# Kernel optimization log

Hardware: AMD Instinct MI355X
Metric: run time of the kernel (lower is better)

## Reference

```python
import jax, jax.numpy as jnp
import numpy as np

B, F, H, E, O = 512, 512, 512, 8, 512  # batch, feature, hidden, experts, out_frame


def setup_inputs() -> dict:
    key = jax.random.key(0)
    ks = jax.random.split(key, 14)
    u = lambda k, shape, s: jax.random.uniform(k, shape, jnp.float32) * s
    return {
        "x": jax.random.normal(ks[0], (B, F), jnp.float32),
        # gating MLP params (torch Linear: y = x @ W.T + b)
        "gw0": u(ks[1], (H, F), 0.04) - 0.02,
        "gb0": jnp.zeros((H,), jnp.float32),
        "gw1": u(ks[2], (H, H), 0.04) - 0.02,
        "gb1": jnp.zeros((H,), jnp.float32),
        "gw2": u(ks[3], (E, H), 0.04) - 0.02,
        "gb2": jnp.zeros((E,), jnp.float32),
        # expert weight/bias banks
        "alpha0": u(ks[4], (E, H, F), 0.01),
        "beta0": jnp.zeros((E, H, 1), jnp.float32),
        "alpha1": u(ks[5], (E, H, H), 0.01),
        "beta1": jnp.zeros((E, H, 1), jnp.float32),
        "alpha2": u(ks[6], (E, O, H), 0.01),
        "beta2": jnp.zeros((E, O, 1), jnp.float32),
    }


def reference(x, gw0, gb0, gw1, gb1, gw2, gb2,
              alpha0, beta0, alpha1, beta1, alpha2, beta2):
    # gating network
    h = jax.nn.elu(x @ gw0.T + gb0)
    h = jax.nn.elu(h @ gw1.T + gb1)
    g = jax.nn.softmax(h @ gw2.T + gb2, axis=1)  # [B, E]

    # per-sample blended weights (sum over experts of gate-scaled expert mats)
    blend_w = lambda a: jnp.einsum('be,ehf->bhf', g, a)
    blend_b = lambda b: jnp.einsum('be,eh->bh', g, b[..., 0])

    # per-sample 3-layer MLP (bmm with vector rhs == batched matvec)
    H1 = jax.nn.elu(jnp.einsum('bhf,bf->bh', blend_w(alpha0), x) + blend_b(beta0))
    H2 = jax.nn.elu(jnp.einsum('bhf,bf->bh', blend_w(alpha1), H1) + blend_b(beta1))
    H3 = jnp.einsum('bof,bf->bo', blend_w(alpha2), H2) + blend_b(beta2)
    return H3
```

## Files before the change

### kernel.cpp

```cpp
#include <hip/hip_runtime.h>
#include <hip/hip_bf16.h>
#include <math.h>

enum { Bq = 512, Fq = 512, Hq = 512, Eq = 8, Oq = 512 };

typedef __attribute__((ext_vector_type(8))) short short8;
typedef __attribute__((ext_vector_type(4))) float floatx4;

static __device__ __forceinline__ unsigned short f2bf(float f) {
  unsigned u = __float_as_uint(f);
  u += 0x7fffu + ((u >> 16) & 1u);
  return (unsigned short)(u >> 16);
}
static __device__ __forceinline__ float bf2f(unsigned short h) {
  return __uint_as_float(((unsigned)h) << 16);
}
static __device__ __forceinline__ float elu1(float v) {
  return v > 0.f ? v : (__expf(v) - 1.f);
}

typedef __attribute__((address_space(1))) const unsigned int gu32;
typedef __attribute__((address_space(3))) unsigned int lu32;
static __device__ __forceinline__ void gld16(const unsigned short* g,
                                             unsigned short* l) {
  __builtin_amdgcn_global_load_lds((gu32*)g, (lu32*)l, 16, 0, 0);
}

static __device__ __forceinline__ int swz(int q, int r) {
  return (q & ~7) | ((q ^ r) & 7);
}

__global__ __launch_bounds__(256) void cvt6_kernel(
    const float* __restrict__ b0, const float* __restrict__ b1,
    const float* __restrict__ b2, unsigned short* __restrict__ db0,
    unsigned short* __restrict__ db1, unsigned short* __restrict__ db2,
    const float* __restrict__ s0, const float* __restrict__ s1,
    const float* __restrict__ s2, unsigned short* __restrict__ ds0,
    unsigned short* __restrict__ ds1, unsigned short* __restrict__ ds2,
    int nb, int ns) {
  int i = blockIdx.x * 256 + threadIdx.x;
  const float4* s;
  unsigned short* d;
  int j;
  if (i < 3 * nb) {
    int seg = i / nb;
    j = i - seg * nb;
    s = (seg == 0) ? (const float4*)b0
      : (seg == 1) ? (const float4*)b1 : (const float4*)b2;
    d = (seg == 0) ? db0 : (seg == 1) ? db1 : db2;
  } else {
    int k = i - 3 * nb;
    if (k >= 3 * ns) return;
    int seg = k / ns;
    j = k - seg * ns;
    s = (seg == 0) ? (const float4*)s0
      : (seg == 1) ? (const float4*)s1 : (const float4*)s2;
    d = (seg == 0) ? ds0 : (seg == 1) ? ds1 : ds2;
  }
  float4 v = s[j];
  ushort4 o;
  o.x = f2bf(v.x); o.y = f2bf(v.y); o.z = f2bf(v.z); o.w = f2bf(v.w);
  *(ushort4*)(d + 4 * (size_t)j) = o;
}

__global__ __launch_bounds__(256) void gating_gemm(
    const unsigned short* __restrict__ A, const unsigned short* __restrict__ W,
    const float* __restrict__ bias, unsigned short* __restrict__ C) {
  __shared__ unsigned short As[32 * 512];
  __shared__ unsigned short Ws[32 * 512];
  const int tid = threadIdx.x;
  const int wave = tid >> 6, lane = tid & 63;
  const int wm = wave >> 1, wn = wave & 1;
  const int lr = lane & 15, lk = lane >> 4;
  const int m0 = blockIdx.y * 32, n0 = blockIdx.x * 32;
#pragma unroll
  for (int i = 0; i < 8; i++) {
    int c = tid + i * 256;
    int r = c >> 6, ql = c & 63;
    gld16(&A[(size_t)(m0 + r) * 512 + swz(ql, r) * 8], &As[(c & ~63) * 8]);
  }
#pragma unroll
  for (int i = 0; i < 8; i++) {
    int c = tid + i * 256;
    int r = c >> 6, ql = c & 63;
    gld16(&W[(size_t)(n0 + r) * 512 + swz(ql, r) * 8], &Ws[(c & ~63) * 8]);
  }
  __syncthreads();
  const int rA = wm * 16 + lr, rB = wn * 16 + lr;
  floatx4 ac[4];
#pragma unroll
  for (int j = 0; j < 4; j++) ac[j] = (floatx4){0.f, 0.f, 0.f, 0.f};
#pragma unroll
  for (int t = 0; t < 4; t++) {
#pragma unroll
    for (int j = 0; j < 4; j++) {
      int q = ((j * 128 + t * 32) >> 3) + lk;
      short8 av = *(const short8*)&As[rA * 512 + swz(q, rA) * 8];
      short8 bv = *(const short8*)&Ws[rB * 512 + swz(q, rB) * 8];
      ac[j] = __builtin_amdgcn_mfma_f32_16x16x32_bf16(av, bv, ac[j], 0, 0, 0);
    }
  }
  floatx4 acc = (ac[0] + ac[1]) + (ac[2] + ac[3]);
  int n = n0 + wn * 16 + lr;
  float bn = bias[n];
#pragma unroll
  for (int r = 0; r < 4; r++) {
    int m = m0 + wm * 16 + lk * 4 + r;
    C[(size_t)m * 512 + n] = f2bf(elu1(acc[r] + bn));
  }
}

template <int FROMP>
__global__ __launch_bounds__(256) void expert_gemm(
    const unsigned short* __restrict__ A,
    const float* __restrict__ Pin,
    const unsigned short* __restrict__ Wb,
    const float* __restrict__ g,
    const float* __restrict__ beta,
    float* __restrict__ Pout) {
  __shared__ unsigned short As[32 * 256];
  __shared__ unsigned short Ws[2][32 * 256];
  const int tid = threadIdx.x;
  const int wave = tid >> 6, lane = tid & 63;
  const int wm = wave >> 1, wn = wave & 1;
  const int lr = lane & 15, lk = lane >> 4;
  const int m0 = blockIdx.y * 32, n0 = blockIdx.x * 32;
  const int kz = blockIdx.z, kbeg = kz * 256;

  if (FROMP) {
#pragma unroll
    for (int i = 0; i < 4; i++) {
      int c = tid + i * 256;
      int r = c >> 5, q = c & 31;
      const float* p0 = Pin + (size_t)(m0 + r) * 512 + kbeg + q * 8;
      const float* p1 = p0 + (size_t)Bq * Hq;
      float4 x0 = *(const float4*)p0, x1 = *(const float4*)(p0 + 4);
      float4 y0 = *(const float4*)p1, y1 = *(const float4*)(p1 + 4);
      short8 o;
      o[0] = (short)f2bf(elu1(x0.x + y0.x));
      o[1] = (short)f2bf(elu1(x0.y + y0.y));
      o[2] = (short)f2bf(elu1(x0.z + y0.z));
      o[3] = (short)f2bf(elu1(x0.w + y0.w));
      o[4] = (short)f2bf(elu1(x1.x + y1.x));
      o[5] = (short)f2bf(elu1(x1.y + y1.y));
      o[6] = (short)f2bf(elu1(x1.z + y1.z));
      o[7] = (short)f2bf(elu1(x1.w + y1.w));
      *(short8*)&As[(r * 32 + swz(q, r)) * 8] = o;
    }
  } else {
#pragma unroll
    for (int i = 0; i < 4; i++) {
      int c = tid + i * 256;
      int r = c >> 5, ql = c & 31;
      gld16(&A[(size_t)(m0 + r) * 512 + kbeg + swz(ql, r) * 8],
            &As[(c & ~63) * 8]);
    }
  }
#pragma unroll
  for (int i = 0; i < 4; i++) {
    int c = tid + i * 256;
    int r = c >> 5, ql = c & 31;
    gld16(&Wb[(size_t)(n0 + r) * 512 + kbeg + swz(ql, r) * 8],
          &Ws[0][(c & ~63) * 8]);
  }
  float g8[4][8];
#pragma unroll
  for (int r = 0; r < 4; r++) {
    int m = m0 + wm * 16 + lk * 4 + r;
    float4 ga = *(const float4*)&g[(size_t)m * 8];
    float4 gb = *(const float4*)&g[(size_t)m * 8 + 4];
    g8[r][0] = ga.x; g8[r][1] = ga.y; g8[r][2] = ga.z; g8[r][3] = ga.w;
    g8[r][4] = gb.x; g8[r][5] = gb.y; g8[r][6] = gb.z; g8[r][7] = gb.w;
  }

  const int rA = wm * 16 + lr, rB = wn * 16 + lr;
  floatx4 fin = {0.f, 0.f, 0.f, 0.f};
#pragma unroll
  for (int e = 0; e < 8; e++) {
    __syncthreads();
    if (e < 7) {
      const unsigned short* Wn = Wb + ((size_t)(e + 1) * 512 + n0) * 512 + kbeg;
#pragma unroll
      for (int i = 0; i < 4; i++) {
        int c = tid + i * 256;
        int r = c >> 5, ql = c & 31;
        gld16(&Wn[(size_t)r * 512 + swz(ql, r) * 8],
              &Ws[(e + 1) & 1][(c & ~63) * 8]);
      }
    }
    const unsigned short* wb = Ws[e & 1];
    floatx4 c0 = {0.f, 0.f, 0.f, 0.f}, c1 = {0.f, 0.f, 0.f, 0.f};
#pragma unroll
    for (int s = 0; s < 8; s++) {
      int q = s * 4 + lk;
      short8 av = *(const short8*)&As[rA * 256 + swz(q, rA) * 8];
      short8 bv = *(const short8*)&wb[rB * 256 + swz(q, rB) * 8];
      if (s & 1)
        c1 = __builtin_amdgcn_mfma_f32_16x16x32_bf16(av, bv, c1, 0, 0, 0);
      else
        c0 = __builtin_amdgcn_mfma_f32_16x16x32_bf16(av, bv, c0, 0, 0, 0);
    }
    floatx4 ae = c0 + c1;
#pragma unroll
    for (int r = 0; r < 4; r++) fin[r] += g8[r][e] * ae[r];
  }

  int n = n0 + wn * 16 + lr;
  if (kz == 0) {
    float bv[8];
#pragma unroll
    for (int e = 0; e < 8; e++) bv[e] = beta[e * 512 + n];
#pragma unroll
    for (int r = 0; r < 4; r++) {
      float bs = 0.f;
#pragma unroll
      for (int e = 0; e < 8; e++) bs += g8[r][e] * bv[e];
      fin[r] += bs;
    }
  }
  float* Po = Pout + (size_t)kz * Bq * Hq;
#pragma unroll
  for (int r = 0; r < 4; r++) {
    int m = m0 + wm * 16 + lk * 4 + r;
    Po[(size_t)m * 512 + n] = fin[r];
  }
}

__global__ __launch_bounds__(64) void gate_kernel(
    const unsigned short* __restrict__ G1,
    const float* __restrict__ gw2,
    const float* __restrict__ gb2,
    float* __restrict__ g) {
  int b = blockIdx.x;
  int lane = threadIdx.x;
  float xv[8];
#pragma unroll
  for (int t = 0; t < 8; t++) xv[t] = bf2f(G1[(size_t)b * Hq + t * 64 + lane]);
  float le[Eq];
#pragma unroll
  for (int e = 0; e < Eq; e++) {
    float p = 0.f;
#pragma unroll
    for (int t = 0; t < 8; t++)
      p += xv[t] * gw2[(size_t)e * Hq + t * 64 + lane];
#pragma unroll
    for (int o = 32; o > 0; o >>= 1) p += __shfl_xor(p, o);
    le[e] = p + gb2[e];
  }
  float m = le[0];
#pragma unroll
  for (int e = 1; e < Eq; e++) m = fmaxf(m, le[e]);
  float s = 0.f;
#pragma unroll
  for (int e = 0; e < Eq; e++) {
    le[e] = __expf(le[e] - m);
    s += le[e];
  }
  float inv = 1.f / s;
  if (lane == 0) {
#pragma unroll
    for (int e = 0; e < Eq; e++) g[(size_t)b * Eq + e] = le[e] * inv;
  }
}

__global__ __launch_bounds__(256) void reduce_final(
    const float* __restrict__ P, float* __restrict__ outf) {
  int idx = blockIdx.x * 256 + threadIdx.x;
  const float4 v0 = ((const float4*)P)[idx];
  const float4 v1 = ((const float4*)(P + (size_t)Bq * Hq))[idx];
  float4 s = {v0.x + v1.x, v0.y + v1.y, v0.z + v1.z, v0.w + v1.w};
  ((float4*)outf)[idx] = s;
}

extern "C" void kernel_launch(void* const* d_in, const int* in_sizes, int n_in,
                              void* d_out, int out_size, void* d_ws,
                              size_t ws_size, hipStream_t stream) {
  const float* x = (const float*)d_in[0];
  const float* gw0 = (const float*)d_in[1];
  const float* gb0 = (const float*)d_in[2];
  const float* gw1 = (const float*)d_in[3];
  const float* gb1 = (const float*)d_in[4];
  const float* gw2 = (const float*)d_in[5];
  const float* gb2 = (const float*)d_in[6];
  const float* alpha0 = (const float*)d_in[7];
  const float* beta0 = (const float*)d_in[8];
  const float* alpha1 = (const float*)d_in[9];
  const float* beta1 = (const float*)d_in[10];
  const float* alpha2 = (const float*)d_in[11];
  const float* beta2 = (const float*)d_in[12];
  float* out = (float*)d_out;

  char* ws = (char*)d_ws;
  auto alloc = [&](size_t bytes) {
    char* p = ws;
    ws += (bytes + 255) & ~(size_t)255;
    return p;
  };
  unsigned short* xb = (unsigned short*)alloc((size_t)Bq * Fq * 2);
  unsigned short* gw0b = (unsigned short*)alloc((size_t)Hq * Fq * 2);
  unsigned short* gw1b = (unsigned short*)alloc((size_t)Hq * Hq * 2);
  unsigned short* a0b = (unsigned short*)alloc((size_t)Eq * Hq * Fq * 2);
  unsigned short* a1b = (unsigned short*)alloc((size_t)Eq * Hq * Hq * 2);
  unsigned short* a2b = (unsigned short*)alloc((size_t)Eq * Oq * Hq * 2);
  unsigned short* G0b = (unsigned short*)alloc((size_t)Bq * Hq * 2);
  unsigned short* G1b = (unsigned short*)alloc((size_t)Bq * Hq * 2);
  float* gates = (float*)alloc((size_t)Bq * Eq * 4);
  float* P1 = (float*)alloc((size_t)2 * Bq * Hq * 4);
  float* P2 = (float*)alloc((size_t)2 * Bq * Hq * 4);

  {
    int nb = (Eq * Hq * Fq) / 4, ns = (Bq * Fq) / 4;
    int total = 3 * nb + 3 * ns;
    cvt6_kernel<<<(total + 255) / 256, 256, 0, stream>>>(
        alpha0, alpha1, alpha2, a0b, a1b, a2b, x, gw0, gw1, xb, gw0b, gw1b,
        nb, ns);
  }

  dim3 gg(16, 16);
  gating_gemm<<<gg, 256, 0, stream>>>(xb, gw0b, gb0, G0b);
  gating_gemm<<<gg, 256, 0, stream>>>(G0b, gw1b, gb1, G1b);

  gate_kernel<<<Bq, 64, 0, stream>>>(G1b, gw2, gb2, gates);

  dim3 ge(16, 16, 2);
  expert_gemm<0><<<ge, 256, 0, stream>>>(xb, nullptr, a0b, gates, beta0, P1);
  expert_gemm<1><<<ge, 256, 0, stream>>>(nullptr, P1, a1b, gates, beta1, P2);
  expert_gemm<1><<<ge, 256, 0, stream>>>(nullptr, P2, a2b, gates, beta2, P1);
  reduce_final<<<(Bq * Hq / 4) / 256, 256, 0, stream>>>(P1, out);
}
```

Before: 137.3 us.

## Retile expert GEMM to 64x64 with split-K 4 and triple-buffered weights

The expert GEMM moves from 32x32 output tiles with split-K 2 to 64x64 tiles with split-K 4. Each wave now computes a 2x2 set of MFMA tiles and keeps its A fragments in registers across all experts. Weight staging uses a three-slot LDS ring with explicit waitcnt and barrier, and gates are staged in LDS. The aim is to cut LDS traffic per MFMA and improve load/compute overlap. In exchange, partial-sum buffers double, so the FROMP prologue and final reduction read twice as many partials, and the grid shrinks to 256 blocks.

After: 142.9 us. 4.0% more time.

```diff
diff --git a/kernel.cpp b/kernel.cpp
--- a/kernel.cpp
+++ b/kernel.cpp
@@ -118,111 +118,141 @@
     const float* __restrict__ g,
     const float* __restrict__ beta,
     float* __restrict__ Pout) {
-  __shared__ unsigned short As[32 * 256];
-  __shared__ unsigned short Ws[2][32 * 256];
+  __shared__ unsigned short As[64 * 128];
+  __shared__ unsigned short Ws[3][64 * 128];
+  __shared__ float gl[64 * 8];
   const int tid = threadIdx.x;
   const int wave = tid >> 6, lane = tid & 63;
   const int wm = wave >> 1, wn = wave & 1;
   const int lr = lane & 15, lk = lane >> 4;
-  const int m0 = blockIdx.y * 32, n0 = blockIdx.x * 32;
-  const int kz = blockIdx.z, kbeg = kz * 256;
+  const int n0 = blockIdx.x * 64, m0 = blockIdx.y * 64;
+  const int kz = blockIdx.z, kbeg = kz * 128;
 
   if (FROMP) {
 #pragma unroll
     for (int i = 0; i < 4; i++) {
       int c = tid + i * 256;
-      int r = c >> 5, q = c & 31;
-      const float* p0 = Pin + (size_t)(m0 + r) * 512 + kbeg + q * 8;
-      const float* p1 = p0 + (size_t)Bq * Hq;
-      float4 x0 = *(const float4*)p0, x1 = *(const float4*)(p0 + 4);
-      float4 y0 = *(const float4*)p1, y1 = *(const float4*)(p1 + 4);
+      int r = c >> 4, q = c & 15;
+      const float* p = Pin + (size_t)(m0 + r) * 512 + kbeg + q * 8;
+      float s0 = 0.f, s1 = 0.f, s2 = 0.f, s3 = 0.f;
+      float s4 = 0.f, s5 = 0.f, s6 = 0.f, s7 = 0.f;
+#pragma unroll
+      for (int z = 0; z < 4; z++) {
+        const float* pz = p + (size_t)z * (Bq * Hq);
+        float4 a = *(const float4*)pz;
+        float4 b = *(const float4*)(pz + 4);
+        s0 += a.x; s1 += a.y; s2 += a.z; s3 += a.w;
+        s4 += b.x; s5 += b.y; s6 += b.z; s7 += b.w;
+      }
       short8 o;
-      o[0] = (short)f2bf(elu1(x0.x + y0.x));
-      o[1] = (short)f2bf(elu1(x0.y + y0.y));
-      o[2] = (short)f2bf(elu1(x0.z + y0.z));
-      o[3] = (short)f2bf(elu1(x0.w + y0.w));
-      o[4] = (short)f2bf(elu1(x1.x + y1.x));
-      o[5] = (short)f2bf(elu1(x1.y + y1.y));
-      o[6] = (short)f2bf(elu1(x1.z + y1.z));
-      o[7] = (short)f2bf(elu1(x1.w + y1.w));
-      *(short8*)&As[(r * 32 + swz(q, r)) * 8] = o;
+      o[0] = (short)f2bf(elu1(s0)); o[1] = (short)f2bf(elu1(s1));
+      o[2] = (short)f2bf(elu1(s2)); o[3] = (short)f2bf(elu1(s3));
+      o[4] = (short)f2bf(elu1(s4)); o[5] = (short)f2bf(elu1(s5));
+      o[6] = (short)f2bf(elu1(s6)); o[7] = (short)f2bf(elu1(s7));
+      *(short8*)&As[(r * 16 + swz(q, r)) * 8] = o;
     }
   } else {
 #pragma unroll
     for (int i = 0; i < 4; i++) {
       int c = tid + i * 256;
-      int r = c >> 5, ql = c & 31;
+      int r = c >> 4, ql = c & 15;
       gld16(&A[(size_t)(m0 + r) * 512 + kbeg + swz(ql, r) * 8],
             &As[(c & ~63) * 8]);
     }
   }
-#pragma unroll
-  for (int i = 0; i < 4; i++) {
-    int c = tid + i * 256;
-    int r = c >> 5, ql = c & 31;
-    gld16(&Wb[(size_t)(n0 + r) * 512 + kbeg + swz(ql, r) * 8],
-          &Ws[0][(c & ~63) * 8]);
-  }
-  float g8[4][8];
-#pragma unroll
-  for (int r = 0; r < 4; r++) {
-    int m = m0 + wm * 16 + lk * 4 + r;
-    float4 ga = *(const float4*)&g[(size_t)m * 8];
-    float4 gb = *(const float4*)&g[(size_t)m * 8 + 4];
-    g8[r][0] = ga.x; g8[r][1] = ga.y; g8[r][2] = ga.z; g8[r][3] = ga.w;
-    g8[r][4] = gb.x; g8[r][5] = gb.y; g8[r][6] = gb.z; g8[r][7] = gb.w;
-  }
-
-  const int rA = wm * 16 + lr, rB = wn * 16 + lr;
-  floatx4 fin = {0.f, 0.f, 0.f, 0.f};
+  if (tid < 128)
+    ((float4*)gl)[tid] = ((const float4*)(g + (size_t)m0 * 8))[tid];
+
+  auto stageW = [&](int e, int b) {
+    const unsigned short* Wp = Wb + ((size_t)e * 512 + n0) * 512 + kbeg;
+#pragma unroll
+    for (int i = 0; i < 4; i++) {
+      int c = tid + i * 256;
+      int r = c >> 4, ql = c & 15;
+      gld16(&Wp[(size_t)r * 512 + swz(ql, r) * 8], &Ws[b][(c & ~63) * 8]);
+    }
+  };
+  stageW(0, 0);
+  stageW(1, 1);
+
+  const int rA0 = wm * 32 + lr, rB0 = wn * 32 + lr;
+  short8 af[2][4];
+  floatx4 fin[2][2];
+#pragma unroll
+  for (int i = 0; i < 2; i++)
+#pragma unroll
+    for (int j = 0; j < 2; j++) fin[i][j] = (floatx4){0.f, 0.f, 0.f, 0.f};
+
 #pragma unroll
   for (int e = 0; e < 8; e++) {
-    __syncthreads();
-    if (e < 7) {
-      const unsigned short* Wn = Wb + ((size_t)(e + 1) * 512 + n0) * 512 + kbeg;
-#pragma unroll
-      for (int i = 0; i < 4; i++) {
-        int c = tid + i * 256;
-        int r = c >> 5, ql = c & 31;
-        gld16(&Wn[(size_t)r * 512 + swz(ql, r) * 8],
-              &Ws[(e + 1) & 1][(c & ~63) * 8]);
-      }
-    }
-    const unsigned short* wb = Ws[e & 1];
-    floatx4 c0 = {0.f, 0.f, 0.f, 0.f}, c1 = {0.f, 0.f, 0.f, 0.f};
-#pragma unroll
-    for (int s = 0; s < 8; s++) {
-      int q = s * 4 + lk;
-      short8 av = *(const short8*)&As[rA * 256 + swz(q, rA) * 8];
-      short8 bv = *(const short8*)&wb[rB * 256 + swz(q, rB) * 8];
-      if (s & 1)
-        c1 = __builtin_amdgcn_mfma_f32_16x16x32_bf16(av, bv, c1, 0, 0, 0);
-      else
-        c0 = __builtin_amdgcn_mfma_f32_16x16x32_bf16(av, bv, c0, 0, 0, 0);
-    }
-    floatx4 ae = c0 + c1;
-#pragma unroll
-    for (int r = 0; r < 4; r++) fin[r] += g8[r][e] * ae[r];
-  }
-
-  int n = n0 + wn * 16 + lr;
-  if (kz == 0) {
-    float bv[8];
-#pragma unroll
-    for (int e = 0; e < 8; e++) bv[e] = beta[e * 512 + n];
-#pragma unroll
-    for (int r = 0; r < 4; r++) {
-      float bs = 0.f;
-#pragma unroll
-      for (int e = 0; e < 8; e++) bs += g8[r][e] * bv[e];
-      fin[r] += bs;
-    }
-  }
+    if (e == 0)
+      __builtin_amdgcn_s_waitcnt(0x0074);
+    else if (e < 7)
+      __builtin_amdgcn_s_waitcnt(0x0F74);
+    else
+      __builtin_amdgcn_s_waitcnt(0x0F70);
+    __builtin_amdgcn_s_barrier();
+    if (e + 2 < 8) stageW(e + 2, (e + 2) % 3);
+    if (e == 0) {
+#pragma unroll
+      for (int i = 0; i < 2; i++) {
+        int r = rA0 + i * 16;
+#pragma unroll
+        for (int t = 0; t < 4; t++)
+          af[i][t] = *(const short8*)&As[r * 128 + swz(t * 4 + lk, r) * 8];
+      }
+    }
+    const unsigned short* wb = Ws[e % 3];
+    floatx4 acc[2][2];
+#pragma unroll
+    for (int i = 0; i < 2; i++)
+#pragma unroll
+      for (int j = 0; j < 2; j++) acc[i][j] = (floatx4){0.f, 0.f, 0.f, 0.f};
+#pragma unroll
+    for (int t = 0; t < 4; t++) {
+      short8 bf[2];
+#pragma unroll
+      for (int j = 0; j < 2; j++) {
+        int r = rB0 + j * 16;
+        bf[j] = *(const short8*)&wb[r * 128 + swz(t * 4 + lk, r) * 8];
+      }
+#pragma unroll
+      for (int i = 0; i < 2; i++)
+#pragma unroll
+        for (int j = 0; j < 2; j++)
+          acc[i][j] = __builtin_amdgcn_mfma_f32_16x16x32_bf16(
+              af[i][t], bf[j], acc[i][j], 0, 0, 0);
+    }
+#pragma unroll
+    for (int i = 0; i < 2; i++) {
+#pragma unroll
+      for (int r = 0; r < 4; r++) {
+        float ge = gl[(wm * 32 + i * 16 + lk * 4 + r) * 8 + e];
+#pragma unroll
+        for (int j = 0; j < 2; j++) fin[i][j][r] += ge * acc[i][j][r];
+      }
+    }
+  }
+
   float* Po = Pout + (size_t)kz * Bq * Hq;
 #pragma unroll
-  for (int r = 0; r < 4; r++) {
-    int m = m0 + wm * 16 + lk * 4 + r;
-    Po[(size_t)m * 512 + n] = fin[r];
+  for (int i = 0; i < 2; i++) {
+#pragma unroll
+    for (int j = 0; j < 2; j++) {
+      int n = n0 + wn * 32 + j * 16 + lr;
+#pragma unroll
+      for (int r = 0; r < 4; r++) {
+        int m = m0 + wm * 32 + i * 16 + lk * 4 + r;
+        float v = fin[i][j][r];
+        if (kz == 0) {
+#pragma unroll
+          for (int e = 0; e < 8; e++)
+            v += gl[(wm * 32 + i * 16 + lk * 4 + r) * 8 + e] *
+                 beta[e * 512 + n];
+        }
+        Po[(size_t)m * 512 + n] = v;
+      }
+    }
   }
 }
 
@@ -266,9 +296,12 @@
 __global__ __launch_bounds__(256) void reduce_final(
     const float* __restrict__ P, float* __restrict__ outf) {
   int idx = blockIdx.x * 256 + threadIdx.x;
-  const float4 v0 = ((const float4*)P)[idx];
-  const float4 v1 = ((const float4*)(P + (size_t)Bq * Hq))[idx];
-  float4 s = {v0.x + v1.x, v0.y + v1.y, v0.z + v1.z, v0.w + v1.w};
+  float4 s = {0.f, 0.f, 0.f, 0.f};
+#pragma unroll
+  for (int z = 0; z < 4; z++) {
+    float4 v = ((const float4*)(P + (size_t)z * Bq * Hq))[idx];
+    s.x += v.x; s.y += v.y; s.z += v.z; s.w += v.w;
+  }
   ((float4*)outf)[idx] = s;
 }
 
@@ -305,8 +338,8 @@
   unsigned short* G0b = (unsigned short*)alloc((size_t)Bq * Hq * 2);
   unsigned short* G1b = (unsigned short*)alloc((size_t)Bq * Hq * 2);
   float* gates = (float*)alloc((size_t)Bq * Eq * 4);
-  float* P1 = (float*)alloc((size_t)2 * Bq * Hq * 4);
-  float* P2 = (float*)alloc((size_t)2 * Bq * Hq * 4);
+  float* P1 = (float*)alloc((size_t)4 * Bq * Hq * 4);
+  float* P2 = (float*)alloc((size_t)4 * Bq * Hq * 4);
 
   {
     int nb = (Eq * Hq * Fq) / 4, ns = (Bq * Fq) / 4;
@@ -322,7 +355,7 @@
 
   gate_kernel<<<Bq, 64, 0, stream>>>(G1b, gw2, gb2, gates);
 
-  dim3 ge(16, 16, 2);
+  dim3 ge(8, 8, 4);
   expert_gemm<0><<<ge, 256, 0, stream>>>(xb, nullptr, a0b, gates, beta0, P1);
   expert_gemm<1><<<ge, 256, 0, stream>>>(nullptr, P1, a1b, gates, beta1, P2);
   expert_gemm<1><<<ge, 256, 0, stream>>>(nullptr, P2, a2b, gates, beta2, P1);
```

## Overlap expert-weight bf16 conversion with gating kernels and fold final reduce into atomics

Applied to the files above, without the earlier changes.

The large alpha-bank fp32-to-bf16 conversion is split across the gating GEMM and gate kernels as extra blocks, so the conversion runs alongside the small gating work instead of in one up-front pass. The gate kernel now packs four rows per 256-thread block and also zeroes the output buffer. The last expert GEMM atomically adds its two K-split partials into the output, which removes the separate reduce kernel. The costs are extra atomic traffic and non-deterministic summation order, and each gating launch now has more blocks and a branch.

After: 136.1 us. No clear change (-0.9%).

```diff
diff --git a/kernel.cpp b/kernel.cpp
--- a/kernel.cpp
+++ b/kernel.cpp
@@ -30,49 +30,42 @@
   return (q & ~7) | ((q ^ r) & 7);
 }
 
-__global__ __launch_bounds__(256) void cvt6_kernel(
-    const float* __restrict__ b0, const float* __restrict__ b1,
-    const float* __restrict__ b2, unsigned short* __restrict__ db0,
-    unsigned short* __restrict__ db1, unsigned short* __restrict__ db2,
-    const float* __restrict__ s0, const float* __restrict__ s1,
-    const float* __restrict__ s2, unsigned short* __restrict__ ds0,
-    unsigned short* __restrict__ ds1, unsigned short* __restrict__ ds2,
-    int nb, int ns) {
-  int i = blockIdx.x * 256 + threadIdx.x;
-  const float4* s;
-  unsigned short* d;
-  int j;
-  if (i < 3 * nb) {
-    int seg = i / nb;
-    j = i - seg * nb;
-    s = (seg == 0) ? (const float4*)b0
-      : (seg == 1) ? (const float4*)b1 : (const float4*)b2;
-    d = (seg == 0) ? db0 : (seg == 1) ? db1 : db2;
-  } else {
-    int k = i - 3 * nb;
-    if (k >= 3 * ns) return;
-    int seg = k / ns;
-    j = k - seg * ns;
-    s = (seg == 0) ? (const float4*)s0
-      : (seg == 1) ? (const float4*)s1 : (const float4*)s2;
-    d = (seg == 0) ? ds0 : (seg == 1) ? ds1 : ds2;
-  }
-  float4 v = s[j];
+static __device__ __forceinline__ void cvt_chunk(const float* __restrict__ src,
+                                                 unsigned short* __restrict__ dst,
+                                                 int chunk, int tid) {
+  int j = chunk * 256 + tid;
+  float4 v = ((const float4*)src)[j];
   ushort4 o;
   o.x = f2bf(v.x); o.y = f2bf(v.y); o.z = f2bf(v.z); o.w = f2bf(v.w);
-  *(ushort4*)(d + 4 * (size_t)j) = o;
-}
-
-__global__ __launch_bounds__(256) void gating_gemm(
+  *(ushort4*)(dst + 4 * (size_t)j) = o;
+}
+
+__global__ __launch_bounds__(256) void cvt_small(
+    const float* __restrict__ s0, const float* __restrict__ s1,
+    const float* __restrict__ s2, unsigned short* __restrict__ d0,
+    unsigned short* __restrict__ d1, unsigned short* __restrict__ d2) {
+  int blk = blockIdx.x;
+  int seg = blk >> 8, c = blk & 255;
+  const float* s = (seg == 0) ? s0 : (seg == 1) ? s1 : s2;
+  unsigned short* d = (seg == 0) ? d0 : (seg == 1) ? d1 : d2;
+  cvt_chunk(s, d, c, threadIdx.x);
+}
+
+__global__ __launch_bounds__(256) void gating_cvt(
     const unsigned short* __restrict__ A, const unsigned short* __restrict__ W,
-    const float* __restrict__ bias, unsigned short* __restrict__ C) {
+    const float* __restrict__ bias, unsigned short* __restrict__ C,
+    const float* __restrict__ asrc, unsigned short* __restrict__ adst) {
+  const int blk = blockIdx.x, tid = threadIdx.x;
+  if (blk >= 256) {
+    cvt_chunk(asrc, adst, blk - 256, tid);
+    return;
+  }
   __shared__ unsigned short As[32 * 512];
   __shared__ unsigned short Ws[32 * 512];
-  const int tid = threadIdx.x;
   const int wave = tid >> 6, lane = tid & 63;
   const int wm = wave >> 1, wn = wave & 1;
   const int lr = lane & 15, lk = lane >> 4;
-  const int m0 = blockIdx.y * 32, n0 = blockIdx.x * 32;
+  const int m0 = (blk >> 4) * 32, n0 = (blk & 15) * 32;
 #pragma unroll
   for (int i = 0; i < 8; i++) {
     int c = tid + i * 256;
@@ -110,7 +103,55 @@
   }
 }
 
-template <int FROMP>
+__global__ __launch_bounds__(256) void gate_fused(
+    const unsigned short* __restrict__ G1,
+    const float* __restrict__ gw2,
+    const float* __restrict__ gb2,
+    float* __restrict__ g,
+    const float* __restrict__ asrc, unsigned short* __restrict__ adst,
+    float* __restrict__ outz) {
+  const int blk = blockIdx.x, tid = threadIdx.x;
+  if (blk >= 384) {
+    cvt_chunk(asrc, adst, blk - 384, tid);
+    return;
+  }
+  if (blk >= 128) {
+    ((float4*)outz)[(blk - 128) * 256 + tid] = (float4){0.f, 0.f, 0.f, 0.f};
+    return;
+  }
+  const int wave = tid >> 6, lane = tid & 63;
+  const int b = blk * 4 + wave;
+  float xv[8];
+#pragma unroll
+  for (int t = 0; t < 8; t++) xv[t] = bf2f(G1[(size_t)b * Hq + t * 64 + lane]);
+  float le[Eq];
+#pragma unroll
+  for (int e = 0; e < Eq; e++) {
+    float p = 0.f;
+#pragma unroll
+    for (int t = 0; t < 8; t++)
+      p += xv[t] * gw2[(size_t)e * Hq + t * 64 + lane];
+#pragma unroll
+    for (int o = 32; o > 0; o >>= 1) p += __shfl_xor(p, o);
+    le[e] = p + gb2[e];
+  }
+  float m = le[0];
+#pragma unroll
+  for (int e = 1; e < Eq; e++) m = fmaxf(m, le[e]);
+  float s = 0.f;
+#pragma unroll
+  for (int e = 0; e < Eq; e++) {
+    le[e] = __expf(le[e] - m);
+    s += le[e];
+  }
+  float inv = 1.f / s;
+  if (lane == 0) {
+#pragma unroll
+    for (int e = 0; e < Eq; e++) g[(size_t)b * Eq + e] = le[e] * inv;
+  }
+}
+
+template <int FROMP, int ATOMIC>
 __global__ __launch_bounds__(256) void expert_gemm(
     const unsigned short* __restrict__ A,
     const float* __restrict__ Pin,
@@ -156,13 +197,16 @@
             &As[(c & ~63) * 8]);
     }
   }
-#pragma unroll
-  for (int i = 0; i < 4; i++) {
-    int c = tid + i * 256;
-    int r = c >> 5, ql = c & 31;
-    gld16(&Wb[(size_t)(n0 + r) * 512 + kbeg + swz(ql, r) * 8],
-          &Ws[0][(c & ~63) * 8]);
-  }
+  auto stageW = [&](int e, int b) {
+    const unsigned short* Wp = Wb + ((size_t)e * 512 + n0) * 512 + kbeg;
+#pragma unroll
+    for (int i = 0; i < 4; i++) {
+      int c = tid + i * 256;
+      int r = c >> 5, ql = c & 31;
+      gld16(&Wp[(size_t)r * 512 + swz(ql, r) * 8], &Ws[b][(c & ~63) * 8]);
+    }
+  };
+  stageW(0, 0);
   float g8[4][8];
 #pragma unroll
   for (int r = 0; r < 4; r++) {
@@ -178,16 +222,7 @@
 #pragma unroll
   for (int e = 0; e < 8; e++) {
     __syncthreads();
-    if (e < 7) {
-      const unsigned short* Wn = Wb + ((size_t)(e + 1) * 512 + n0) * 512 + kbeg;
-#pragma unroll
-      for (int i = 0; i < 4; i++) {
-        int c = tid + i * 256;
-        int r = c >> 5, ql = c & 31;
-        gld16(&Wn[(size_t)r * 512 + swz(ql, r) * 8],
-              &Ws[(e + 1) & 1][(c & ~63) * 8]);
-      }
-    }
+    if (e < 7) stageW(e + 1, (e + 1) & 1);
     const unsigned short* wb = Ws[e & 1];
     floatx4 c0 = {0.f, 0.f, 0.f, 0.f}, c1 = {0.f, 0.f, 0.f, 0.f};
 #pragma unroll
@@ -218,58 +253,20 @@
       fin[r] += bs;
     }
   }
-  float* Po = Pout + (size_t)kz * Bq * Hq;
-#pragma unroll
-  for (int r = 0; r < 4; r++) {
-    int m = m0 + wm * 16 + lk * 4 + r;
-    Po[(size_t)m * 512 + n] = fin[r];
-  }
-}
-
-__global__ __launch_bounds__(64) void gate_kernel(
-    const unsigned short* __restrict__ G1,
-    const float* __restrict__ gw2,
-    const float* __restrict__ gb2,
-    float* __restrict__ g) {
-  int b = blockIdx.x;
-  int lane = threadIdx.x;
-  float xv[8];
-#pragma unroll
-  for (int t = 0; t < 8; t++) xv[t] = bf2f(G1[(size_t)b * Hq + t * 64 + lane]);
-  float le[Eq];
-#pragma unroll
-  for (int e = 0; e < Eq; e++) {
-    float p = 0.f;
-#pragma unroll
-    for (int t = 0; t < 8; t++)
-      p += xv[t] * gw2[(size_t)e * Hq + t * 64 + lane];
-#pragma unroll
-    for (int o = 32; o > 0; o >>= 1) p += __shfl_xor(p, o);
-    le[e] = p + gb2[e];
-  }
-  float m = le[0];
-#pragma unroll
-  for (int e = 1; e < Eq; e++) m = fmaxf(m, le[e]);
-  float s = 0.f;
-#pragma unroll
-  for (int e = 0; e < Eq; e++) {
-    le[e] = __expf(le[e] - m);
-    s += le[e];
-  }
-  float inv = 1.f / s;
-  if (lane == 0) {
-#pragma unroll
-    for (int e = 0; e < Eq; e++) g[(size_t)b * Eq + e] = le[e] * inv;
-  }
-}
-
-__global__ __launch_bounds__(256) void reduce_final(
-    const float* __restrict__ P, float* __restrict__ outf) {
-  int idx = blockIdx.x * 256 + threadIdx.x;
-  const float4 v0 = ((const float4*)P)[idx];
-  const float4 v1 = ((const float4*)(P + (size_t)Bq * Hq))[idx];
-  float4 s = {v0.x + v1.x, v0.y + v1.y, v0.z + v1.z, v0.w + v1.w};
-  ((float4*)outf)[idx] = s;
+  if (ATOMIC) {
+#pragma unroll
+    for (int r = 0; r < 4; r++) {
+      int m = m0 + wm * 16 + lk * 4 + r;
+      atomicAdd(&Pout[(size_t)m * 512 + n], fin[r]);
+    }
+  } else {
+    float* Po = Pout + (size_t)kz * Bq * Hq;
+#pragma unroll
+    for (int r = 0; r < 4; r++) {
+      int m = m0 + wm * 16 + lk * 4 + r;
+      Po[(size_t)m * 512 + n] = fin[r];
+    }
+  }
 }
 
 extern "C" void kernel_launch(void* const* d_in, const int* in_sizes, int n_in,
@@ -308,23 +305,15 @@
   float* P1 = (float*)alloc((size_t)2 * Bq * Hq * 4);
   float* P2 = (float*)alloc((size_t)2 * Bq * Hq * 4);
 
-  {
-    int nb = (Eq * Hq * Fq) / 4, ns = (Bq * Fq) / 4;
-    int total = 3 * nb + 3 * ns;
-    cvt6_kernel<<<(total + 255) / 256, 256, 0, stream>>>(
-        alpha0, alpha1, alpha2, a0b, a1b, a2b, x, gw0, gw1, xb, gw0b, gw1b,
-        nb, ns);
-  }
-
-  dim3 gg(16, 16);
-  gating_gemm<<<gg, 256, 0, stream>>>(xb, gw0b, gb0, G0b);
-  gating_gemm<<<gg, 256, 0, stream>>>(G0b, gw1b, gb1, G1b);
-
-  gate_kernel<<<Bq, 64, 0, stream>>>(G1b, gw2, gb2, gates);
+  cvt_small<<<768, 256, 0, stream>>>(x, gw0, gw1, xb, gw0b, gw1b);
+
+  gating_cvt<<<2304, 256, 0, stream>>>(xb, gw0b, gb0, G0b, alpha0, a0b);
+  gating_cvt<<<2304, 256, 0, stream>>>(G0b, gw1b, gb1, G1b, alpha1, a1b);
+
+  gate_fused<<<2432, 256, 0, stream>>>(G1b, gw2, gb2, gates, alpha2, a2b, out);
 
   dim3 ge(16, 16, 2);
-  expert_gemm<0><<<ge, 256, 0, stream>>>(xb, nullptr, a0b, gates, beta0, P1);
-  expert_gemm<1><<<ge, 256, 0, stream>>>(nullptr, P1, a1b, gates, beta1, P2);
-  expert_gemm<1><<<ge, 256, 0, stream>>>(nullptr, P2, a2b, gates, beta2, P1);
-  reduce_final<<<(Bq * Hq / 4) / 256, 256, 0, stream>>>(P1, out);
-}
+  expert_gemm<0, 0><<<ge, 256, 0, stream>>>(xb, nullptr, a0b, gates, beta0, P1);
+  expert_gemm<1, 0><<<ge, 256, 0, stream>>>(nullptr, P1, a1b, gates, beta1, P2);
+  expert_gemm<1, 1><<<ge, 256, 0, stream>>>(nullptr, P2, a2b, gates, beta2, out);
+}
```
